# Optimization experiments

Measured on AMD Instinct MI355X. Metric: run time of the kernel, lower is better.

Reference implementation:

```python
import jax, jax.numpy as jnp
import numpy as np

N_CLIENTS = 1_000_000
N_ITEMS = 100_000
D = 128          # embedding_dim (in_feats)
H = 128          # output_size (h_feats)
N_NODES = 100_000
N_EDGES = 1_600_000


def setup_inputs() -> dict:
    key = jax.random.key(0)
    ks = jax.random.split(key, 12)
    f32 = jnp.float32
    return {
        # TwoPartEmbedding tables
        "client_table": jax.random.normal(ks[0], (N_CLIENTS, D), dtype=f32) * 0.02,
        "item_table": jax.random.normal(ks[1], (N_ITEMS, D), dtype=f32) * 0.02,
        # SAGEConv layer 1 (in_feats -> h_feats)
        "W_self1": jax.random.normal(ks[2], (D, H), dtype=f32) * (1.0 / np.sqrt(D)),
        "W_neigh1": jax.random.normal(ks[3], (D, H), dtype=f32) * (1.0 / np.sqrt(D)),
        "b1": jnp.zeros((H,), dtype=f32),
        # SAGEConv layer 2 (h_feats -> h_feats)
        "W_self2": jax.random.normal(ks[4], (H, H), dtype=f32) * (1.0 / np.sqrt(H)),
        "W_neigh2": jax.random.normal(ks[5], (H, H), dtype=f32) * (1.0 / np.sqrt(H)),
        "b2": jnp.zeros((H,), dtype=f32),
        # subgraph data
        "node_ids": jax.random.randint(ks[6], (N_NODES,), 0, N_CLIENTS + N_ITEMS),
        "src": jax.random.randint(ks[7], (N_EDGES,), 0, N_NODES),
        "dst": jax.random.randint(ks[8], (N_EDGES,), 0, N_NODES),
    }


def _two_part_embedding(node_ids, client_table, item_table):
    # IDs < N_CLIENTS index the client table; the rest (offset) index the item table.
    is_client = node_ids < N_CLIENTS
    cx = client_table[jnp.where(is_client, node_ids, 0)]              # [N, D]
    ix = item_table[jnp.where(is_client, 0, node_ids - N_CLIENTS)]    # [N, D]
    return jnp.where(is_client[:, None], cx, ix)


def _sage_layer(x, src, dst, W_self, W_neigh, b):
    # DGL SAGEConv, mean aggregator: gather src features, segment-mean onto dst.
    msg = x[src]  # [E, d]
    agg = jax.ops.segment_sum(msg, dst, num_segments=N_NODES)
    deg = jax.ops.segment_sum(jnp.ones((src.shape[0],), dtype=x.dtype), dst,
                              num_segments=N_NODES)
    h_neigh = agg / jnp.maximum(deg, 1.0)[:, None]
    return x @ W_self + h_neigh @ W_neigh + b


def reference(client_table, item_table, W_self1, W_neigh1, b1,
              W_self2, W_neigh2, b2, node_ids, src, dst):
    x = _two_part_embedding(node_ids, client_table, item_table)       # [N, D]
    h = jax.nn.relu(_sage_layer(x, src, dst, W_self1, W_neigh1, b1))  # [N, H]
    out = _sage_layer(h, src, dst, W_self2, W_neigh2, b2)             # [N, H]
    return out
```

## Files before the change

kernel.cpp:

```cpp
#include <hip/hip_runtime.h>


#define N_CLIENTS 1000000
#define N_NODES   100000
#define N_EDGES   1600000
#define DCAP      64

typedef unsigned short u16;
typedef unsigned int   u32;
typedef __bf16  bf16x8 __attribute__((ext_vector_type(8)));
typedef float   f32x4  __attribute__((ext_vector_type(4)));

__device__ __forceinline__ u16 f2bf(float f) {
    union { float f; u32 i; } c; c.f = f;
    u32 r = c.i + 0x7FFFu + ((c.i >> 16) & 1u);
    return (u16)(r >> 16);
}
__device__ __forceinline__ float2 bfpair(u32 u) {
    union { u32 i; float f; } lo, hi;
    lo.i = u << 16; hi.i = u & 0xFFFF0000u;
    return make_float2(lo.f, hi.f);
}

__global__ __launch_bounds__(256) void front_kernel(
    const float* __restrict__ client, const float* __restrict__ item,
    const int* __restrict__ ids,
    const int* __restrict__ src, const int* __restrict__ dst,
    const float* __restrict__ W0, const float* __restrict__ W1,
    const float* __restrict__ W2, const float* __restrict__ W3,
    u16* __restrict__ Xb, int* __restrict__ cnt, int* __restrict__ bucket,
    u16* __restrict__ Wt)
{
    int b = blockIdx.x;
    if (b < 6250) {
        int e = b * 256 + threadIdx.x;
        int d = dst[e];
        int pos = atomicAdd(&cnt[d], 1);
        if (pos < DCAP) bucket[(size_t)d * DCAP + pos] = src[e];
    } else if (b < 18750) {
        int t = (b - 6250) * 256 + threadIdx.x;
        int node = t >> 5, j = t & 31;
        if (node >= N_NODES) return;
        int id = ids[node];
        const float4* row = (id < N_CLIENTS)
            ? (const float4*)(client + (size_t)id * 128)
            : (const float4*)(item + (size_t)(id - N_CLIENTS) * 128);
        float4 v = row[j];
        uint2 o;
        o.x = ((u32)f2bf(v.y) << 16) | f2bf(v.x);
        o.y = ((u32)f2bf(v.w) << 16) | f2bf(v.z);
        *(uint2*)(Xb + (size_t)node * 128 + j * 4) = o;
    } else {
        int i = (b - 18750) * 256 + threadIdx.x;
        int mat = i >> 14, k = (i >> 7) & 127, n = i & 127;
        const float* W = mat == 0 ? W0 : mat == 1 ? W1 : mat == 2 ? W2 : W3;
        Wt[mat * 16384 + n * 128 + k] = f2bf(W[k * 128 + n]);
    }
}

#define GB 64
__global__ __launch_bounds__(256) void layer_kernel(
    const u16* __restrict__ Xin,
    const int* __restrict__ cnt, const int* __restrict__ bucket,
    const u16* __restrict__ Wts, const u16* __restrict__ Wtn,
    const float* __restrict__ bias,
    u16* __restrict__ OUTb, float* __restrict__ OUTf, int relu)
{
    __shared__ u16 wlds[128 * 144];
    __shared__ u16 hnl[GB * 136];
    int tid = threadIdx.x;
    int w = tid >> 6, lane = tid & 63;
    int m = lane & 15, q = lane >> 4;
    int r0 = blockIdx.x * GB;
    int rowa = r0 + w * 16 + m;
    int rowc = rowa < N_NODES ? rowa : N_NODES - 1;

    for (int i = tid; i < 128 * 16; i += 256) {
        int n = i >> 4, c8 = i & 15;
        *(uint4*)&wlds[n * 144 + c8 * 8] = *(const uint4*)(Wts + n * 128 + c8 * 8);
    }

    bf16x8 ax[4];
    #pragma unroll
    for (int kc = 0; kc < 4; ++kc)
        ax[kc] = *(const bf16x8*)(Xin + (size_t)rowc * 128 + kc * 32 + q * 8);

    for (int rr = 0; rr < 16; ++rr) {
        int drow = r0 + w * 16 + rr;
        int dv = drow < N_NODES ? drow : N_NODES - 1;
        dv = __builtin_amdgcn_readfirstlane(dv);
        int d = cnt[dv];
        int dc = d < DCAP ? d : DCAP;
        const int* bk = bucket + (size_t)dv * DCAP;
        float sx = 0.f, sy = 0.f;
        int e = 0;
        for (; e + 8 <= dc; e += 8) {
            u32 u[8];
            #pragma unroll
            for (int z = 0; z < 8; ++z) {
                int s = bk[e + z];
                u[z] = *(const u32*)(Xin + (size_t)s * 128 + lane * 2);
            }
            #pragma unroll
            for (int z = 0; z < 8; ++z) {
                float2 v = bfpair(u[z]);
                sx += v.x; sy += v.y;
            }
        }
        for (; e < dc; ++e) {
            float2 v = bfpair(*(const u32*)(Xin + (size_t)bk[e] * 128 + lane * 2));
            sx += v.x; sy += v.y;
        }
        float inv = 1.0f / fmaxf((float)d, 1.0f);
        *(u32*)&hnl[(w * 16 + rr) * 136 + lane * 2] =
            ((u32)f2bf(sy * inv) << 16) | f2bf(sx * inv);
    }
    __syncthreads();

    bf16x8 ah[4];
    #pragma unroll
    for (int kc = 0; kc < 4; ++kc)
        ah[kc] = *(const bf16x8*)&hnl[(w * 16 + m) * 136 + kc * 32 + q * 8];

    f32x4 acc[8];
    #pragma unroll
    for (int t = 0; t < 8; ++t) {
        float bv = bias[t * 16 + m];
        acc[t] = (f32x4){bv, bv, bv, bv};
    }

    #pragma unroll
    for (int kc = 0; kc < 4; ++kc)
        #pragma unroll
        for (int t = 0; t < 8; ++t) {
            bf16x8 bfr = *(const bf16x8*)&wlds[(t * 16 + m) * 144 + kc * 32 + q * 8];
            acc[t] = __builtin_amdgcn_mfma_f32_16x16x32_bf16(ax[kc], bfr, acc[t], 0, 0, 0);
        }
    __syncthreads();

    for (int i = tid; i < 128 * 16; i += 256) {
        int n = i >> 4, c8 = i & 15;
        *(uint4*)&wlds[n * 144 + c8 * 8] = *(const uint4*)(Wtn + n * 128 + c8 * 8);
    }
    __syncthreads();
    #pragma unroll
    for (int kc = 0; kc < 4; ++kc)
        #pragma unroll
        for (int t = 0; t < 8; ++t) {
            bf16x8 bfr = *(const bf16x8*)&wlds[(t * 16 + m) * 144 + kc * 32 + q * 8];
            acc[t] = __builtin_amdgcn_mfma_f32_16x16x32_bf16(ah[kc], bfr, acc[t], 0, 0, 0);
        }

    #pragma unroll
    for (int t = 0; t < 8; ++t) {
        int col = t * 16 + m;
        #pragma unroll
        for (int r = 0; r < 4; ++r) {
            int row = r0 + w * 16 + q * 4 + r;
            if (row < N_NODES) {
                float v = acc[t][r];
                if (relu) v = fmaxf(v, 0.f);
                if (OUTb) OUTb[(size_t)row * 128 + col] = f2bf(v);
                else      OUTf[(size_t)row * 128 + col] = v;
            }
        }
    }
}

extern "C" void kernel_launch(void* const* d_in, const int* in_sizes, int n_in,
                              void* d_out, int out_size, void* d_ws, size_t ws_size,
                              hipStream_t stream) {
    const float* client = (const float*)d_in[0];
    const float* item   = (const float*)d_in[1];
    const float* Ws1    = (const float*)d_in[2];
    const float* Wn1    = (const float*)d_in[3];
    const float* b1     = (const float*)d_in[4];
    const float* Ws2    = (const float*)d_in[5];
    const float* Wn2    = (const float*)d_in[6];
    const float* b2     = (const float*)d_in[7];
    const int* node_ids = (const int*)d_in[8];
    const int* src      = (const int*)d_in[9];
    const int* dst      = (const int*)d_in[10];
    float* out = (float*)d_out;

    char* ws = (char*)d_ws;
    u16* xb     = (u16*)ws;
    u16* hb     = (u16*)(ws + 25600000);
    int* cnt    = (int*)(ws + 51200000);
    int* bucket = (int*)(ws + 51600000);
    u16* Wt     = (u16*)(ws + 77200000);

    hipMemsetAsync(cnt, 0, N_NODES * sizeof(int), stream);
    front_kernel<<<19006, 256, 0, stream>>>(client, item, node_ids, src, dst,
                                            Ws1, Wn1, Ws2, Wn2,
                                            xb, cnt, bucket, Wt);
    layer_kernel<<<1563, 256, 0, stream>>>(xb, cnt, bucket, Wt, Wt + 16384,
                                           b1, hb, (float*)nullptr, 1);
    layer_kernel<<<1563, 256, 0, stream>>>(hb, cnt, bucket, Wt + 32768, Wt + 49152,
                                           b2, (u16*)nullptr, out, 0);
}
```

Measured before the change: 1.025 ms.

## Fuse front and layer kernels into one cooperative persistent kernel with grid syncs

Merges the memset, front gather/bucketing kernel and both SAGE layer kernels into a single cooperative launch. Grid-wide syncs separate the phases, and blocks loop persistently over tiles. The neighbour-list loads are also restructured: each wave loads one bucket row into registers, prefetches the next row, and broadcasts source indices with shuffles instead of scalar loads. This aims to cut launch and inter-kernel gaps and to hide bucket-load latency, at the cost of a smaller grid, grid.sync overhead and the weights being reloaded into shared memory per tile. A fallback multi-kernel path is kept.

```diff
diff --git a/kernel.cpp b/kernel.cpp
--- a/kernel.cpp
+++ b/kernel.cpp
@@ -1,10 +1,14 @@
 #include <hip/hip_runtime.h>
+#include <hip/hip_cooperative_groups.h>
+
+namespace cg = cooperative_groups;
 
 
 #define N_CLIENTS 1000000
 #define N_NODES   100000
 #define N_EDGES   1600000
 #define DCAP      64
+#define NTILES    1563
 
 typedef unsigned short u16;
 typedef unsigned int   u32;
@@ -22,7 +26,7 @@
     return make_float2(lo.f, hi.f);
 }
 
-__global__ __launch_bounds__(256) void front_kernel(
+__device__ __forceinline__ void phase_front(
     const float* __restrict__ client, const float* __restrict__ item,
     const int* __restrict__ ids,
     const int* __restrict__ src, const int* __restrict__ dst,
@@ -31,16 +35,15 @@
     u16* __restrict__ Xb, int* __restrict__ cnt, int* __restrict__ bucket,
     u16* __restrict__ Wt)
 {
-    int b = blockIdx.x;
-    if (b < 6250) {
-        int e = b * 256 + threadIdx.x;
+    int gtid = blockIdx.x * 256 + threadIdx.x;
+    int gs = gridDim.x * 256;
+    for (int e = gtid; e < N_EDGES; e += gs) {
         int d = dst[e];
         int pos = atomicAdd(&cnt[d], 1);
         if (pos < DCAP) bucket[(size_t)d * DCAP + pos] = src[e];
-    } else if (b < 18750) {
-        int t = (b - 6250) * 256 + threadIdx.x;
+    }
+    for (int t = gtid; t < N_NODES * 32; t += gs) {
         int node = t >> 5, j = t & 31;
-        if (node >= N_NODES) return;
         int id = ids[node];
         const float4* row = (id < N_CLIENTS)
             ? (const float4*)(client + (size_t)id * 128)
@@ -50,121 +53,167 @@
         o.x = ((u32)f2bf(v.y) << 16) | f2bf(v.x);
         o.y = ((u32)f2bf(v.w) << 16) | f2bf(v.z);
         *(uint2*)(Xb + (size_t)node * 128 + j * 4) = o;
-    } else {
-        int i = (b - 18750) * 256 + threadIdx.x;
+    }
+    for (int i = gtid; i < 65536; i += gs) {
         int mat = i >> 14, k = (i >> 7) & 127, n = i & 127;
         const float* W = mat == 0 ? W0 : mat == 1 ? W1 : mat == 2 ? W2 : W3;
         Wt[mat * 16384 + n * 128 + k] = f2bf(W[k * 128 + n]);
     }
 }
 
-#define GB 64
-__global__ __launch_bounds__(256) void layer_kernel(
+__device__ void layer_tiles(
     const u16* __restrict__ Xin,
     const int* __restrict__ cnt, const int* __restrict__ bucket,
     const u16* __restrict__ Wts, const u16* __restrict__ Wtn,
     const float* __restrict__ bias,
-    u16* __restrict__ OUTb, float* __restrict__ OUTf, int relu)
-{
-    __shared__ u16 wlds[128 * 144];
-    __shared__ u16 hnl[GB * 136];
+    u16* __restrict__ OUTb, float* __restrict__ OUTf, int relu,
+    u16* wlds, u16* hnl)
+{
     int tid = threadIdx.x;
     int w = tid >> 6, lane = tid & 63;
     int m = lane & 15, q = lane >> 4;
-    int r0 = blockIdx.x * GB;
-    int rowa = r0 + w * 16 + m;
-    int rowc = rowa < N_NODES ? rowa : N_NODES - 1;
-
-    for (int i = tid; i < 128 * 16; i += 256) {
-        int n = i >> 4, c8 = i & 15;
-        *(uint4*)&wlds[n * 144 + c8 * 8] = *(const uint4*)(Wts + n * 128 + c8 * 8);
-    }
-
-    bf16x8 ax[4];
-    #pragma unroll
-    for (int kc = 0; kc < 4; ++kc)
-        ax[kc] = *(const bf16x8*)(Xin + (size_t)rowc * 128 + kc * 32 + q * 8);
-
-    for (int rr = 0; rr < 16; ++rr) {
-        int drow = r0 + w * 16 + rr;
-        int dv = drow < N_NODES ? drow : N_NODES - 1;
-        dv = __builtin_amdgcn_readfirstlane(dv);
-        int d = cnt[dv];
-        int dc = d < DCAP ? d : DCAP;
-        const int* bk = bucket + (size_t)dv * DCAP;
-        float sx = 0.f, sy = 0.f;
-        int e = 0;
-        for (; e + 8 <= dc; e += 8) {
-            u32 u[8];
+    for (int tile = blockIdx.x; tile < NTILES; tile += gridDim.x) {
+        int r0 = tile * 64;
+        for (int i = tid; i < 128 * 16; i += 256) {
+            int n = i >> 4, c8 = i & 15;
+            *(uint4*)&wlds[n * 144 + c8 * 8] = *(const uint4*)(Wts + n * 128 + c8 * 8);
+        }
+        int rowa = r0 + w * 16 + m;
+        int rowc = rowa < N_NODES ? rowa : N_NODES - 1;
+        bf16x8 ax[4];
+        #pragma unroll
+        for (int kc = 0; kc < 4; ++kc)
+            ax[kc] = *(const bf16x8*)(Xin + (size_t)rowc * 128 + kc * 32 + q * 8);
+
+        int crow = r0 + w * 16 + (lane & 15);
+        int crowc = crow < N_NODES ? crow : N_NODES - 1;
+        int dall = cnt[crowc];
+        int rv0 = r0 + w * 16;
+        int dv0 = rv0 < N_NODES ? rv0 : N_NODES - 1;
+        int srcs = bucket[(size_t)dv0 * DCAP + lane];
+        for (int rr = 0; rr < 16; ++rr) {
+            int d = __shfl(dall, rr);
+            int dc = d < DCAP ? d : DCAP;
+            int nsrcs = 0;
+            if (rr < 15) {
+                int nr = r0 + w * 16 + rr + 1;
+                int nv = nr < N_NODES ? nr : N_NODES - 1;
+                nsrcs = bucket[(size_t)nv * DCAP + lane];
+            }
+            float sx = 0.f, sy = 0.f;
+            int e = 0;
+            for (; e + 8 <= dc; e += 8) {
+                u32 uu[8];
+                #pragma unroll
+                for (int z = 0; z < 8; ++z) {
+                    int s = __shfl(srcs, e + z);
+                    uu[z] = *(const u32*)(Xin + (size_t)s * 128 + lane * 2);
+                }
+                #pragma unroll
+                for (int z = 0; z < 8; ++z) {
+                    float2 v = bfpair(uu[z]);
+                    sx += v.x; sy += v.y;
+                }
+            }
+            for (; e < dc; ++e) {
+                int s = __shfl(srcs, e);
+                float2 v = bfpair(*(const u32*)(Xin + (size_t)s * 128 + lane * 2));
+                sx += v.x; sy += v.y;
+            }
+            float inv = 1.0f / fmaxf((float)d, 1.0f);
+            *(u32*)&hnl[(w * 16 + rr) * 136 + lane * 2] =
+                ((u32)f2bf(sy * inv) << 16) | f2bf(sx * inv);
+            srcs = nsrcs;
+        }
+        __syncthreads();
+
+        bf16x8 ah[4];
+        #pragma unroll
+        for (int kc = 0; kc < 4; ++kc)
+            ah[kc] = *(const bf16x8*)&hnl[(w * 16 + m) * 136 + kc * 32 + q * 8];
+
+        f32x4 acc[8];
+        #pragma unroll
+        for (int t = 0; t < 8; ++t) {
+            float bv = bias[t * 16 + m];
+            acc[t] = (f32x4){bv, bv, bv, bv};
+        }
+        #pragma unroll
+        for (int kc = 0; kc < 4; ++kc)
             #pragma unroll
-            for (int z = 0; z < 8; ++z) {
-                int s = bk[e + z];
-                u[z] = *(const u32*)(Xin + (size_t)s * 128 + lane * 2);
-            }
+            for (int t = 0; t < 8; ++t) {
+                bf16x8 bfr = *(const bf16x8*)&wlds[(t * 16 + m) * 144 + kc * 32 + q * 8];
+                acc[t] = __builtin_amdgcn_mfma_f32_16x16x32_bf16(ax[kc], bfr, acc[t], 0, 0, 0);
+            }
+        __syncthreads();
+        for (int i = tid; i < 128 * 16; i += 256) {
+            int n = i >> 4, c8 = i & 15;
+            *(uint4*)&wlds[n * 144 + c8 * 8] = *(const uint4*)(Wtn + n * 128 + c8 * 8);
+        }
+        __syncthreads();
+        #pragma unroll
+        for (int kc = 0; kc < 4; ++kc)
             #pragma unroll
-            for (int z = 0; z < 8; ++z) {
-                float2 v = bfpair(u[z]);
-                sx += v.x; sy += v.y;
-            }
-        }
-        for (; e < dc; ++e) {
-            float2 v = bfpair(*(const u32*)(Xin + (size_t)bk[e] * 128 + lane * 2));
-            sx += v.x; sy += v.y;
-        }
-        float inv = 1.0f / fmaxf((float)d, 1.0f);
-        *(u32*)&hnl[(w * 16 + rr) * 136 + lane * 2] =
-            ((u32)f2bf(sy * inv) << 16) | f2bf(sx * inv);
-    }
-    __syncthreads();
-
-    bf16x8 ah[4];
-    #pragma unroll
-    for (int kc = 0; kc < 4; ++kc)
-        ah[kc] = *(const bf16x8*)&hnl[(w * 16 + m) * 136 + kc * 32 + q * 8];
-
-    f32x4 acc[8];
-    #pragma unroll
-    for (int t = 0; t < 8; ++t) {
-        float bv = bias[t * 16 + m];
-        acc[t] = (f32x4){bv, bv, bv, bv};
-    }
-
-    #pragma unroll
-    for (int kc = 0; kc < 4; ++kc)
+            for (int t = 0; t < 8; ++t) {
+                bf16x8 bfr = *(const bf16x8*)&wlds[(t * 16 + m) * 144 + kc * 32 + q * 8];
+                acc[t] = __builtin_amdgcn_mfma_f32_16x16x32_bf16(ah[kc], bfr, acc[t], 0, 0, 0);
+            }
         #pragma unroll
         for (int t = 0; t < 8; ++t) {
-            bf16x8 bfr = *(const bf16x8*)&wlds[(t * 16 + m) * 144 + kc * 32 + q * 8];
-            acc[t] = __builtin_amdgcn_mfma_f32_16x16x32_bf16(ax[kc], bfr, acc[t], 0, 0, 0);
-        }
-    __syncthreads();
-
-    for (int i = tid; i < 128 * 16; i += 256) {
-        int n = i >> 4, c8 = i & 15;
-        *(uint4*)&wlds[n * 144 + c8 * 8] = *(const uint4*)(Wtn + n * 128 + c8 * 8);
-    }
-    __syncthreads();
-    #pragma unroll
-    for (int kc = 0; kc < 4; ++kc)
-        #pragma unroll
-        for (int t = 0; t < 8; ++t) {
-            bf16x8 bfr = *(const bf16x8*)&wlds[(t * 16 + m) * 144 + kc * 32 + q * 8];
-            acc[t] = __builtin_amdgcn_mfma_f32_16x16x32_bf16(ah[kc], bfr, acc[t], 0, 0, 0);
-        }
-
-    #pragma unroll
-    for (int t = 0; t < 8; ++t) {
-        int col = t * 16 + m;
-        #pragma unroll
-        for (int r = 0; r < 4; ++r) {
-            int row = r0 + w * 16 + q * 4 + r;
-            if (row < N_NODES) {
-                float v = acc[t][r];
-                if (relu) v = fmaxf(v, 0.f);
-                if (OUTb) OUTb[(size_t)row * 128 + col] = f2bf(v);
-                else      OUTf[(size_t)row * 128 + col] = v;
-            }
-        }
-    }
+            int col = t * 16 + m;
+            #pragma unroll
+            for (int r = 0; r < 4; ++r) {
+                int row = r0 + w * 16 + q * 4 + r;
+                if (row < N_NODES) {
+                    float v = acc[t][r];
+                    if (relu) v = fmaxf(v, 0.f);
+                    if (OUTb) OUTb[(size_t)row * 128 + col] = f2bf(v);
+                    else      OUTf[(size_t)row * 128 + col] = v;
+                }
+            }
+        }
+        __syncthreads();
+    }
+}
+
+__global__ __launch_bounds__(256, 3) void mega_kernel(
+    const float* client, const float* item,
+    const float* W0, const float* W1, const float* W2, const float* W3,
+    const float* b1, const float* b2,
+    const int* ids, const int* src, const int* dst,
+    u16* xb, u16* hb, int* cnt, int* bucket, u16* Wt, float* out)
+{
+    __shared__ u16 wlds[128 * 144];
+    __shared__ u16 hnl[64 * 136];
+    cg::grid_group grid = cg::this_grid();
+    int gtid = blockIdx.x * 256 + threadIdx.x;
+    int gs = gridDim.x * 256;
+    for (int i = gtid; i < N_NODES; i += gs) cnt[i] = 0;
+    grid.sync();
+    phase_front(client, item, ids, src, dst, W0, W1, W2, W3, xb, cnt, bucket, Wt);
+    grid.sync();
+    layer_tiles(xb, cnt, bucket, Wt, Wt + 16384, b1, hb, (float*)nullptr, 1, wlds, hnl);
+    grid.sync();
+    layer_tiles(hb, cnt, bucket, Wt + 32768, Wt + 49152, b2, (u16*)nullptr, out, 0, wlds, hnl);
+}
+
+__global__ __launch_bounds__(256) void front_kernel(
+    const float* client, const float* item,
+    const float* W0, const float* W1, const float* W2, const float* W3,
+    const int* ids, const int* src, const int* dst,
+    u16* xb, int* cnt, int* bucket, u16* Wt)
+{
+    phase_front(client, item, ids, src, dst, W0, W1, W2, W3, xb, cnt, bucket, Wt);
+}
+
+__global__ __launch_bounds__(256, 3) void layer_kernel(
+    const u16* Xin, const int* cnt, const int* bucket,
+    const u16* Wts, const u16* Wtn, const float* bias,
+    u16* OUTb, float* OUTf, int relu)
+{
+    __shared__ u16 wlds[128 * 144];
+    __shared__ u16 hnl[64 * 136];
+    layer_tiles(Xin, cnt, bucket, Wts, Wtn, bias, OUTb, OUTf, relu, wlds, hnl);
 }
 
 extern "C" void kernel_launch(void* const* d_in, const int* in_sizes, int n_in,
@@ -190,12 +239,39 @@
     int* bucket = (int*)(ws + 51600000);
     u16* Wt     = (u16*)(ws + 77200000);
 
+    static int coopGrid = -2;
+    if (coopGrid == -2) {
+        int maxb = 0;
+        if (hipOccupancyMaxActiveBlocksPerMultiprocessor(
+                &maxb, (const void*)mega_kernel, 256, 0) == hipSuccess && maxb > 0) {
+            coopGrid = maxb * 256;
+            if (coopGrid > 2048) coopGrid = 2048;
+        } else {
+            coopGrid = -1;
+        }
+    }
+
+    if (coopGrid > 0) {
+        void* args[] = {
+            (void*)&client, (void*)&item,
+            (void*)&Ws1, (void*)&Wn1, (void*)&Ws2, (void*)&Wn2,
+            (void*)&b1, (void*)&b2,
+            (void*)&node_ids, (void*)&src, (void*)&dst,
+            (void*)&xb, (void*)&hb, (void*)&cnt, (void*)&bucket,
+            (void*)&Wt, (void*)&out
+        };
+        hipError_t err = hipLaunchCooperativeKernel(
+            (const void*)mega_kernel, dim3(coopGrid), dim3(256),
+            args, 0, stream);
+        if (err == hipSuccess) return;
+        coopGrid = -1;
+    }
+
     hipMemsetAsync(cnt, 0, N_NODES * sizeof(int), stream);
-    front_kernel<<<19006, 256, 0, stream>>>(client, item, node_ids, src, dst,
-                                            Ws1, Wn1, Ws2, Wn2,
-                                            xb, cnt, bucket, Wt);
-    layer_kernel<<<1563, 256, 0, stream>>>(xb, cnt, bucket, Wt, Wt + 16384,
-                                           b1, hb, (float*)nullptr, 1);
-    layer_kernel<<<1563, 256, 0, stream>>>(hb, cnt, bucket, Wt + 32768, Wt + 49152,
-                                           b2, (u16*)nullptr, out, 0);
-}
+    front_kernel<<<2048, 256, 0, stream>>>(client, item, Ws1, Wn1, Ws2, Wn2,
+                                           node_ids, src, dst, xb, cnt, bucket, Wt);
+    layer_kernel<<<NTILES, 256, 0, stream>>>(xb, cnt, bucket, Wt, Wt + 16384,
+                                             b1, hb, (float*)nullptr, 1);
+    layer_kernel<<<NTILES, 256, 0, stream>>>(hb, cnt, bucket, Wt + 32768, Wt + 49152,
+                                             b2, (u16*)nullptr, out, 0);
+}
```

Result: slower. 1.410 ms (+37.6%).
